# Kernel tuning notes

Measured on AMD Instinct MI355X. Metric: run time of the kernel, lower is better.

Reference implementation:

```python
import jax, jax.numpy as jnp
import numpy as np

B, C, N = 4, 512, 4096
CQK = C // 8

def setup_inputs() -> dict:
    key = jax.random.key(0)
    ks = jax.random.split(key, 8)
    s = 0.02  # weight init scale
    return {
        "x": jax.random.normal(ks[0], (B, C, N), dtype=jnp.float32),
        "Wq": jax.random.normal(ks[1], (CQK, C), dtype=jnp.float32) * s,
        "bq": jax.random.normal(ks[2], (CQK,), dtype=jnp.float32) * s,
        "Wk": jax.random.normal(ks[3], (CQK, C), dtype=jnp.float32) * s,
        "bk": jax.random.normal(ks[4], (CQK,), dtype=jnp.float32) * s,
        "Wv": jax.random.normal(ks[5], (C, C), dtype=jnp.float32) * s,
        "bv": jax.random.normal(ks[6], (C,), dtype=jnp.float32) * s,
        "gamma": jax.random.normal(ks[7], (1,), dtype=jnp.float32),
    }

def reference(x, Wq, bq, Wk, bk, Wv, bv, gamma):
    # pointwise Conv1d == per-point matmul: [B,C,N] -> [B,Cout,N]
    q = jnp.einsum('oc,bcn->bon', Wq, x) + bq[None, :, None]   # [B,CQK,N]
    k = jnp.einsum('oc,bcn->bon', Wk, x) + bk[None, :, None]   # [B,CQK,N]
    v = jnp.einsum('oc,bcn->bon', Wv, x) + bv[None, :, None]   # [B,C,N]
    # attention[b,i,j] = sum_c q[b,c,i] * k[b,c,j]  (unscaled, non-causal)
    attn = jnp.einsum('bci,bcj->bij', q, k)                    # [B,N,N]
    attn = jax.nn.softmax(attn, axis=-1)
    # out[b,c,i] = sum_j v[b,c,j] * attn[b,i,j]
    out = jnp.einsum('bcj,bij->bci', v, attn)                  # [B,C,N]
    return gamma[0] * out + x
```

## Files before the change

### kernel.cpp

```cpp
#include <hip/hip_runtime.h>
#include <math.h>

#define B_ 4
#define C_ 512
#define N_ 4096
#define LOG2E 1.44269504088896f

typedef __attribute__((ext_vector_type(8))) short s8v;
typedef __attribute__((ext_vector_type(4))) float f4v;

#define MF32(a, b, c) __builtin_amdgcn_mfma_f32_16x16x32_bf16(a, b, c, 0, 0, 0)

#if defined(__has_builtin) && __has_builtin(__builtin_amdgcn_exp2f)
#define EXP2(x) __builtin_amdgcn_exp2f(x)
#else
#define EXP2(x) exp2f(x)
#endif

#define BARRIER_LDS() do {                                   \
    __builtin_amdgcn_sched_barrier(0);                       \
    asm volatile("s_waitcnt lgkmcnt(0)" ::: "memory");       \
    __builtin_amdgcn_s_barrier();                            \
    __builtin_amdgcn_sched_barrier(0);                       \
} while (0)

static __device__ __forceinline__ ushort f2bf(float f) {
    unsigned u = __float_as_uint(f);
    u += 0x7FFFu + ((u >> 16) & 1u);
    return (ushort)(u >> 16);
}
static __device__ __forceinline__ unsigned pack2bf(float a, float b) {
    unsigned ua = __float_as_uint(a); ua += 0x7FFFu + ((ua >> 16) & 1u);
    unsigned ub = __float_as_uint(b); ub += 0x7FFFu + ((ub >> 16) & 1u);
    return (ua >> 16) | (ub & 0xffff0000u);
}

__global__ __launch_bounds__(256) void wconv_kernel(
    const float* __restrict__ Wq, const float* __restrict__ Wk,
    const float* __restrict__ Wv, ushort* __restrict__ Wb)
{
    const int row = blockIdx.x;
    const float* src = row < 64 ? Wq + (size_t)row * C_
                     : row < 128 ? Wk + (size_t)(row - 64) * C_
                     : Wv + (size_t)(row - 128) * C_;
    const int t2 = threadIdx.x * 2;
    float2 v = *(const float2*)&src[t2];
    ushort2 o; o.x = f2bf(v.x); o.y = f2bf(v.y);
    *(ushort2*)&Wb[(size_t)row * C_ + t2] = o;
}

__global__ __launch_bounds__(512, 2) void qkv_fused(
    const float* __restrict__ x, const ushort* __restrict__ Wb,
    const float* __restrict__ bq, const float* __restrict__ bk,
    const float* __restrict__ bv,
    ushort* __restrict__ qT, ushort* __restrict__ kT, ushort* __restrict__ vB)
{
    extern __shared__ ushort Xs[];

    const int tid = threadIdx.x, w = tid >> 6, lane = tid & 63;
    const int li = lane & 15, qd = lane >> 4;
    const int n0 = blockIdx.x * 64, b = blockIdx.y;

    #pragma unroll
    for (int r = 0; r < 16; ++r) {
        const int f = r * 512 + tid;
        const int c = f >> 4;
        const int nch = f & 15;
        float4 v = *(const float4*)&x[((size_t)b * C_ + c) * N_ + n0 + nch * 4];
        const int n = nch * 4;
        Xs[((n + 0) * 512 + c) ^ (((n + 0) & 7) << 3)] = f2bf(v.x);
        Xs[((n + 1) * 512 + c) ^ (((n + 1) & 7) << 3)] = f2bf(v.y);
        Xs[((n + 2) * 512 + c) ^ (((n + 2) & 7) << 3)] = f2bf(v.z);
        Xs[((n + 3) * 512 + c) ^ (((n + 3) & 7) << 3)] = f2bf(v.w);
    }
    __syncthreads();

    const int rb0 = w * 80;
    const ushort* wrow[5];
    #pragma unroll
    for (int ot = 0; ot < 5; ++ot)
        wrow[ot] = Wb + (size_t)(rb0 + ot * 16 + li) * C_ + qd * 8;

    f4v acc[5][4];
    #pragma unroll
    for (int ot = 0; ot < 5; ++ot)
        #pragma unroll
        for (int nt = 0; nt < 4; ++nt)
            acc[ot][nt] = (f4v){0.f, 0.f, 0.f, 0.f};

    s8v awc[5], awn[5];
    #pragma unroll
    for (int ot = 0; ot < 5; ++ot)
        awc[ot] = *(const s8v*)(wrow[ot]);

    #pragma unroll 1
    for (int kc = 0; kc < C_; kc += 32) {
        const int kn = (kc + 32 < C_) ? kc + 32 : 0;
        #pragma unroll
        for (int ot = 0; ot < 5; ++ot)
            awn[ot] = *(const s8v*)(wrow[ot] + kn);

        s8v bx[4];
        #pragma unroll
        for (int nt = 0; nt < 4; ++nt) {
            const int n = nt * 16 + li;
            bx[nt] = *(const s8v*)&Xs[((n * 512) + kc + qd * 8) ^ ((li & 7) << 3)];
        }

        #pragma unroll
        for (int ot = 0; ot < 5; ++ot) {
            if (rb0 + ot * 16 >= 128) {
                #pragma unroll
                for (int nt = 0; nt < 4; ++nt)
                    acc[ot][nt] = MF32(bx[nt], awc[ot], acc[ot][nt]);
            } else {
                #pragma unroll
                for (int nt = 0; nt < 4; ++nt)
                    acc[ot][nt] = MF32(awc[ot], bx[nt], acc[ot][nt]);
            }
        }
        #pragma unroll
        for (int ot = 0; ot < 5; ++ot) awc[ot] = awn[ot];
    }

    #pragma unroll
    for (int ot = 0; ot < 5; ++ot) {
        const int rb = rb0 + ot * 16;
        if (rb < 128) {
            ushort* dst = rb < 64 ? qT : kT;
            const float* bias = rb < 64 ? bq : bk;
            const int ob = (rb < 64 ? rb : rb - 64) + qd * 4;
            const float sc = rb < 64 ? LOG2E : 1.0f;
            #pragma unroll
            for (int nt = 0; nt < 4; ++nt) {
                const int n = n0 + nt * 16 + li;
                ushort4 o;
                o.x = f2bf((acc[ot][nt][0] + bias[ob + 0]) * sc);
                o.y = f2bf((acc[ot][nt][1] + bias[ob + 1]) * sc);
                o.z = f2bf((acc[ot][nt][2] + bias[ob + 2]) * sc);
                o.w = f2bf((acc[ot][nt][3] + bias[ob + 3]) * sc);
                *(ushort4*)&dst[((size_t)b * N_ + n) * 64 + ob] = o;
            }
        } else {
            const int c = rb - 128 + li;
            const float bb = bv[c];
            #pragma unroll
            for (int nt = 0; nt < 4; ++nt) {
                const int n = n0 + nt * 16 + qd * 4;
                ushort4 o;
                o.x = f2bf(acc[ot][nt][0] + bb);
                o.y = f2bf(acc[ot][nt][1] + bb);
                o.z = f2bf(acc[ot][nt][2] + bb);
                o.w = f2bf(acc[ot][nt][3] + bb);
                *(ushort4*)&vB[((size_t)b * C_ + c) * N_ + n] = o;
            }
        }
    }
}

__device__ __forceinline__ void pv_chunk(
    const ushort* __restrict__ Pr, int li, int qd, int cidx,
    const s8v* vf, f4v (&acc)[4][8])
{
    const int sw = li & 7;
    #pragma unroll
    for (int h = 0; h < 2; ++h) {
        s8v pf[4];
        #pragma unroll
        for (int g = 0; g < 4; ++g)
            pf[g] = *(const s8v*)&Pr[(size_t)((h * 4 + g) * 16 + li) * 128
                                     + (((cidx * 4 + qd) ^ sw) << 3)];
        #pragma unroll
        for (int ct = 0; ct < 4; ++ct)
            #pragma unroll
            for (int g = 0; g < 4; ++g)
                acc[ct][h * 4 + g] = MF32(vf[ct], pf[g], acc[ct][h * 4 + g]);
    }
}

__device__ __forceinline__ void s_phase(
    s8v ck0, s8v ck1, const s8v (&qf)[8][2], float (&lp)[8],
    ushort* __restrict__ Pw, int li, int qd, int chunkbase)
{
    const int off = (qd & 1) * 4;
    const int sw = li & 7;
    #pragma unroll
    for (int h = 0; h < 2; ++h) {
        f4v sac[4];
        #pragma unroll
        for (int g = 0; g < 4; ++g) {
            const int it = h * 4 + g;
            sac[g] = (f4v){0.f, 0.f, 0.f, 0.f};
            sac[g] = MF32(ck0, qf[it][0], sac[g]);
            sac[g] = MF32(ck1, qf[it][1], sac[g]);
        }
        #pragma unroll
        for (int g = 0; g < 4; ++g) {
            const int it = h * 4 + g;
            const float p0 = EXP2(sac[g][0]);
            const float p1 = EXP2(sac[g][1]);
            const float p2 = EXP2(sac[g][2]);
            const float p3 = EXP2(sac[g][3]);
            lp[it] += (p0 + p1) + (p2 + p3);
            uint2 u; u.x = pack2bf(p0, p1); u.y = pack2bf(p2, p3);
            *(uint2*)&Pw[(size_t)(it * 16 + li) * 128
                         + ((chunkbase ^ sw) << 3) + off] = u;
        }
    }
}

__global__ __launch_bounds__(512, 2) void attn_mfma(
    const ushort* __restrict__ qT, const ushort* __restrict__ kT,
    const ushort* __restrict__ vB, const float* __restrict__ x,
    const float* __restrict__ gamma, float* __restrict__ out)
{
    extern __shared__ char smem[];
    ushort* Pb0 = (ushort*)smem;
    ushort* Pb1 = (ushort*)(smem + 32768);
    float*  l_s = (float*)(smem + 65536);

    const int tid = threadIdx.x, w = tid >> 6, lane = tid & 63;
    const int li = lane & 15, qd = lane >> 4;
    const int wg = blockIdx.x;
    const int i_base = (wg >> 3) * 128;
    const int combo = wg & 7;
    const int b = combo >> 1;
    const int c_base = (combo & 1) * 256;

    const ushort* qTb = qT + (size_t)b * N_ * 64;
    const ushort* kTb = kT + (size_t)b * N_ * 64;
    const ushort* vBb = vB + (size_t)b * C_ * N_;

    if (w < 4) {
        s8v qf[8][2];
        #pragma unroll
        for (int it = 0; it < 8; ++it)
            #pragma unroll
            for (int ks = 0; ks < 2; ++ks)
                qf[it][ks] = *(const s8v*)&qTb[(size_t)(i_base + it * 16 + li) * 64 + ks * 32 + qd * 8];
        float lp[8] = {0.f, 0.f, 0.f, 0.f, 0.f, 0.f, 0.f, 0.f};

        const ushort* kptrA = kTb + (size_t)(w * 32 + li) * 64 + qd * 8;
        const ushort* kptrB = kTb + (size_t)(w * 32 + 16 + li) * 64 + qd * 8;
        const int cbA = w * 4 + (qd >> 1);
        const int cbB = w * 4 + 2 + (qd >> 1);

        s8v ka0 = *(const s8v*)(kptrA);
        s8v ka1 = *(const s8v*)(kptrA + 32);
        s8v kb0 = *(const s8v*)(kptrB);
        s8v kb1 = *(const s8v*)(kptrB + 32);
        s8v na0 = *(const s8v*)(kptrA + (size_t)128 * 64);
        s8v na1 = *(const s8v*)(kptrA + (size_t)128 * 64 + 32);
        s8v nb0 = *(const s8v*)(kptrB + (size_t)128 * 64);
        s8v nb1 = *(const s8v*)(kptrB + (size_t)128 * 64 + 32);
        s_phase(ka0, ka1, qf, lp, Pb0, li, qd, cbA);
        s_phase(kb0, kb1, qf, lp, Pb0, li, qd, cbB);
        BARRIER_LDS();

        #pragma unroll 1
        for (int t = 1; t < N_ / 128; ++t) {
            ushort* Pw = ((t - 1) & 1) ? Pb0 : Pb1;
            const size_t jnext = (t + 1 < N_ / 128) ? (size_t)(t + 1) * 128 : 0;
            s8v ca0 = na0, ca1 = na1, cb0 = nb0, cb1 = nb1;
            na0 = *(const s8v*)(kptrA + jnext * 64);
            na1 = *(const s8v*)(kptrA + jnext * 64 + 32);
            nb0 = *(const s8v*)(kptrB + jnext * 64);
            nb1 = *(const s8v*)(kptrB + jnext * 64 + 32);
            s_phase(ca0, ca1, qf, lp, Pw, li, qd, cbA);
            s_phase(cb0, cb1, qf, lp, Pw, li, qd, cbB);
            BARRIER_LDS();
        }

        #pragma unroll
        for (int it = 0; it < 8; ++it) {
            lp[it] += __shfl_xor(lp[it], 16, 64);
            lp[it] += __shfl_xor(lp[it], 32, 64);
        }
        if (qd == 0) {
            #pragma unroll
            for (int it = 0; it < 8; ++it) l_s[w * 128 + it * 16 + li] = lp[it];
        }
        BARRIER_LDS();
    } else {
        const int w2c = w - 4;
        f4v acc[4][8];
        #pragma unroll
        for (int ct = 0; ct < 4; ++ct)
            #pragma unroll
            for (int it = 0; it < 8; ++it)
                acc[ct][it] = (f4v){0.f, 0.f, 0.f, 0.f};

        const ushort* vptr[4];
        #pragma unroll
        for (int ct = 0; ct < 4; ++ct)
            vptr[ct] = vBb + (size_t)(c_base + w2c * 64 + ct * 16 + li) * N_ + qd * 8;

        s8v vcur[8];
        #pragma unroll
        for (int ch = 0; ch < 2; ++ch)
            #pragma unroll
            for (int ct = 0; ct < 4; ++ct)
                vcur[ch * 4 + ct] = *(const s8v*)(vptr[ct] + ch * 32);
        BARRIER_LDS();

        #pragma unroll 1
        for (int t = 1; t < N_ / 128; ++t) {
            const ushort* Pr = ((t - 1) & 1) ? Pb1 : Pb0;
            const size_t jprev = (size_t)(t - 1) * 128;
            const size_t jcur  = (size_t)t * 128;

            __builtin_amdgcn_s_setprio(1);
            s8v vlt0[4], vlt1[4], vnx[8];
            #pragma unroll
            for (int ct = 0; ct < 4; ++ct)
                vlt0[ct] = *(const s8v*)(vptr[ct] + jprev + 2 * 32);
            pv_chunk(Pr, li, qd, 0, &vcur[0], acc);
            #pragma unroll
            for (int ct = 0; ct < 4; ++ct)
                vlt1[ct] = *(const s8v*)(vptr[ct] + jprev + 3 * 32);
            pv_chunk(Pr, li, qd, 1, &vcur[4], acc);
            #pragma unroll
            for (int ct = 0; ct < 4; ++ct)
                vnx[ct] = *(const s8v*)(vptr[ct] + jcur);
            pv_chunk(Pr, li, qd, 2, vlt0, acc);
            #pragma unroll
            for (int ct = 0; ct < 4; ++ct)
                vnx[4 + ct] = *(const s8v*)(vptr[ct] + jcur + 32);
            pv_chunk(Pr, li, qd, 3, vlt1, acc);
            __builtin_amdgcn_s_setprio(0);

            #pragma unroll
            for (int k = 0; k < 8; ++k) vcur[k] = vnx[k];
            BARRIER_LDS();
        }

        {
            const ushort* Pr = ((N_ / 128 - 1) & 1) ? Pb1 : Pb0;
            const size_t jprev = (size_t)(N_ / 128 - 1) * 128;
            s8v vlt0[4], vlt1[4];
            #pragma unroll
            for (int ct = 0; ct < 4; ++ct)
                vlt0[ct] = *(const s8v*)(vptr[ct] + jprev + 2 * 32);
            pv_chunk(Pr, li, qd, 0, &vcur[0], acc);
            #pragma unroll
            for (int ct = 0; ct < 4; ++ct)
                vlt1[ct] = *(const s8v*)(vptr[ct] + jprev + 3 * 32);
            pv_chunk(Pr, li, qd, 1, &vcur[4], acc);
            pv_chunk(Pr, li, qd, 2, vlt0, acc);
            pv_chunk(Pr, li, qd, 3, vlt1, acc);
        }
        BARRIER_LDS();

        float inv[8];
        #pragma unroll
        for (int it = 0; it < 8; ++it) {
            float t = 0.f;
            #pragma unroll
            for (int ww = 0; ww < 4; ++ww) t += l_s[ww * 128 + it * 16 + li];
            inv[it] = 1.0f / t;
        }

        const float g = gamma[0];
        #pragma unroll
        for (int ct = 0; ct < 4; ++ct)
            #pragma unroll
            for (int it = 0; it < 8; ++it) {
                const int i = i_base + it * 16 + li;
                #pragma unroll
                for (int r = 0; r < 4; ++r) {
                    const int c = c_base + w2c * 64 + ct * 16 + qd * 4 + r;
                    const size_t off = ((size_t)b * C_ + c) * N_ + i;
                    out[off] = g * acc[ct][it][r] * inv[it] + x[off];
                }
            }
    }
}

extern "C" void kernel_launch(void* const* d_in, const int* in_sizes, int n_in,
                              void* d_out, int out_size, void* d_ws, size_t ws_size,
                              hipStream_t stream)
{
    const float* x     = (const float*)d_in[0];
    const float* Wq    = (const float*)d_in[1];
    const float* bq    = (const float*)d_in[2];
    const float* Wk    = (const float*)d_in[3];
    const float* bk    = (const float*)d_in[4];
    const float* Wv    = (const float*)d_in[5];
    const float* bv    = (const float*)d_in[6];
    const float* gamma = (const float*)d_in[7];
    float* out = (float*)d_out;

    ushort* vB = (ushort*)d_ws;
    ushort* qT = vB + (size_t)B_ * C_ * N_;
    ushort* kT = qT + (size_t)B_ * N_ * 64;
    ushort* Wb = kT + (size_t)B_ * N_ * 64;

    wconv_kernel<<<dim3(640), 256, 0, stream>>>(Wq, Wk, Wv, Wb);
    qkv_fused<<<dim3(N_ / 64, B_), 512, 65536, stream>>>(x, Wb, bq, bk, bv, qT, kT, vB);
    attn_mfma<<<dim3((N_ / 128) * 2 * B_), 512, 69632, stream>>>(qT, kT, vB, x, gamma, out);
}
```

Measured before the change: 212.3 us.

## Double the attention key tile to 256 and rotate V register prefetch

Measured after the change: 205.4 us. 3.3% less time.

```diff
diff --git a/kernel.cpp b/kernel.cpp
--- a/kernel.cpp
+++ b/kernel.cpp
@@ -168,7 +168,7 @@
         s8v pf[4];
         #pragma unroll
         for (int g = 0; g < 4; ++g)
-            pf[g] = *(const s8v*)&Pr[(size_t)((h * 4 + g) * 16 + li) * 128
+            pf[g] = *(const s8v*)&Pr[(size_t)((h * 4 + g) * 16 + li) * 256
                                      + (((cidx * 4 + qd) ^ sw) << 3)];
         #pragma unroll
         for (int ct = 0; ct < 4; ++ct)
@@ -203,7 +203,7 @@
             const float p3 = EXP2(sac[g][3]);
             lp[it] += (p0 + p1) + (p2 + p3);
             uint2 u; u.x = pack2bf(p0, p1); u.y = pack2bf(p2, p3);
-            *(uint2*)&Pw[(size_t)(it * 16 + li) * 128
+            *(uint2*)&Pw[(size_t)(it * 16 + li) * 256
                          + ((chunkbase ^ sw) << 3) + off] = u;
         }
     }
@@ -216,8 +216,8 @@
 {
     extern __shared__ char smem[];
     ushort* Pb0 = (ushort*)smem;
-    ushort* Pb1 = (ushort*)(smem + 32768);
-    float*  l_s = (float*)(smem + 65536);
+    ushort* Pb1 = (ushort*)(smem + 65536);
+    float*  l_s = (float*)smem;
 
     const int tid = threadIdx.x, w = tid >> 6, lane = tid & 63;
     const int li = lane & 15, qd = lane >> 4;
@@ -231,6 +231,8 @@
     const ushort* kTb = kT + (size_t)b * N_ * 64;
     const ushort* vBb = vB + (size_t)b * C_ * N_;
 
+    const int NT = N_ / 256;
+
     if (w < 4) {
         s8v qf[8][2];
         #pragma unroll
@@ -240,34 +242,44 @@
                 qf[it][ks] = *(const s8v*)&qTb[(size_t)(i_base + it * 16 + li) * 64 + ks * 32 + qd * 8];
         float lp[8] = {0.f, 0.f, 0.f, 0.f, 0.f, 0.f, 0.f, 0.f};
 
-        const ushort* kptrA = kTb + (size_t)(w * 32 + li) * 64 + qd * 8;
-        const ushort* kptrB = kTb + (size_t)(w * 32 + 16 + li) * 64 + qd * 8;
-        const int cbA = w * 4 + (qd >> 1);
-        const int cbB = w * 4 + 2 + (qd >> 1);
-
-        s8v ka0 = *(const s8v*)(kptrA);
-        s8v ka1 = *(const s8v*)(kptrA + 32);
-        s8v kb0 = *(const s8v*)(kptrB);
-        s8v kb1 = *(const s8v*)(kptrB + 32);
-        s8v na0 = *(const s8v*)(kptrA + (size_t)128 * 64);
-        s8v na1 = *(const s8v*)(kptrA + (size_t)128 * 64 + 32);
-        s8v nb0 = *(const s8v*)(kptrB + (size_t)128 * 64);
-        s8v nb1 = *(const s8v*)(kptrB + (size_t)128 * 64 + 32);
-        s_phase(ka0, ka1, qf, lp, Pb0, li, qd, cbA);
-        s_phase(kb0, kb1, qf, lp, Pb0, li, qd, cbB);
+        const ushort* kp[4];
+        int cb[4];
+        #pragma unroll
+        for (int s = 0; s < 4; ++s) {
+            kp[s] = kTb + (size_t)(w * 64 + s * 16 + li) * 64 + qd * 8;
+            cb[s] = w * 8 + s * 2 + (qd >> 1);
+        }
+
+        s8v kn0[4], kn1[4];
+        {
+            s8v kc0[4], kc1[4];
+            #pragma unroll
+            for (int s = 0; s < 4; ++s) {
+                kc0[s] = *(const s8v*)(kp[s]);
+                kc1[s] = *(const s8v*)(kp[s] + 32);
+            }
+            #pragma unroll
+            for (int s = 0; s < 4; ++s) {
+                kn0[s] = *(const s8v*)(kp[s] + (size_t)256 * 64);
+                kn1[s] = *(const s8v*)(kp[s] + (size_t)256 * 64 + 32);
+            }
+            #pragma unroll
+            for (int s = 0; s < 4; ++s)
+                s_phase(kc0[s], kc1[s], qf, lp, Pb0, li, qd, cb[s]);
+        }
         BARRIER_LDS();
 
         #pragma unroll 1
-        for (int t = 1; t < N_ / 128; ++t) {
+        for (int t = 1; t < NT; ++t) {
             ushort* Pw = ((t - 1) & 1) ? Pb0 : Pb1;
-            const size_t jnext = (t + 1 < N_ / 128) ? (size_t)(t + 1) * 128 : 0;
-            s8v ca0 = na0, ca1 = na1, cb0 = nb0, cb1 = nb1;
-            na0 = *(const s8v*)(kptrA + jnext * 64);
-            na1 = *(const s8v*)(kptrA + jnext * 64 + 32);
-            nb0 = *(const s8v*)(kptrB + jnext * 64);
-            nb1 = *(const s8v*)(kptrB + jnext * 64 + 32);
-            s_phase(ca0, ca1, qf, lp, Pw, li, qd, cbA);
-            s_phase(cb0, cb1, qf, lp, Pw, li, qd, cbB);
+            const size_t jnext = (t + 1 < NT) ? (size_t)(t + 1) * 256 : 0;
+            #pragma unroll
+            for (int s = 0; s < 4; ++s) {
+                s8v c0 = kn0[s], c1 = kn1[s];
+                kn0[s] = *(const s8v*)(kp[s] + jnext * 64);
+                kn1[s] = *(const s8v*)(kp[s] + jnext * 64 + 32);
+                s_phase(c0, c1, qf, lp, Pw, li, qd, cb[s]);
+            }
             BARRIER_LDS();
         }
 
@@ -295,59 +307,49 @@
         for (int ct = 0; ct < 4; ++ct)
             vptr[ct] = vBb + (size_t)(c_base + w2c * 64 + ct * 16 + li) * N_ + qd * 8;
 
-        s8v vcur[8];
-        #pragma unroll
-        for (int ch = 0; ch < 2; ++ch)
+        s8v vr[2][4];
+        #pragma unroll
+        for (int sl = 0; sl < 2; ++sl)
             #pragma unroll
             for (int ct = 0; ct < 4; ++ct)
-                vcur[ch * 4 + ct] = *(const s8v*)(vptr[ct] + ch * 32);
+                vr[sl][ct] = *(const s8v*)(vptr[ct] + sl * 32);
         BARRIER_LDS();
 
         #pragma unroll 1
-        for (int t = 1; t < N_ / 128; ++t) {
+        for (int t = 1; t < NT; ++t) {
             const ushort* Pr = ((t - 1) & 1) ? Pb1 : Pb0;
-            const size_t jprev = (size_t)(t - 1) * 128;
-            const size_t jcur  = (size_t)t * 128;
+            const size_t jprev = (size_t)(t - 1) * 256;
+            const size_t jcur  = (size_t)t * 256;
 
             __builtin_amdgcn_s_setprio(1);
-            s8v vlt0[4], vlt1[4], vnx[8];
-            #pragma unroll
-            for (int ct = 0; ct < 4; ++ct)
-                vlt0[ct] = *(const s8v*)(vptr[ct] + jprev + 2 * 32);
-            pv_chunk(Pr, li, qd, 0, &vcur[0], acc);
-            #pragma unroll
-            for (int ct = 0; ct < 4; ++ct)
-                vlt1[ct] = *(const s8v*)(vptr[ct] + jprev + 3 * 32);
-            pv_chunk(Pr, li, qd, 1, &vcur[4], acc);
-            #pragma unroll
-            for (int ct = 0; ct < 4; ++ct)
-                vnx[ct] = *(const s8v*)(vptr[ct] + jcur);
-            pv_chunk(Pr, li, qd, 2, vlt0, acc);
-            #pragma unroll
-            for (int ct = 0; ct < 4; ++ct)
-                vnx[4 + ct] = *(const s8v*)(vptr[ct] + jcur + 32);
-            pv_chunk(Pr, li, qd, 3, vlt1, acc);
+            #pragma unroll
+            for (int c = 0; c < 8; ++c) {
+                pv_chunk(Pr, li, qd, c, vr[c & 1], acc);
+                const size_t jld = (c + 2 < 8) ? jprev + (size_t)(c + 2) * 32
+                                               : jcur + (size_t)(c + 2 - 8) * 32;
+                #pragma unroll
+                for (int ct = 0; ct < 4; ++ct)
+                    vr[c & 1][ct] = *(const s8v*)(vptr[ct] + jld);
+            }
             __builtin_amdgcn_s_setprio(0);
-
-            #pragma unroll
-            for (int k = 0; k < 8; ++k) vcur[k] = vnx[k];
             BARRIER_LDS();
         }
 
         {
-            const ushort* Pr = ((N_ / 128 - 1) & 1) ? Pb1 : Pb0;
-            const size_t jprev = (size_t)(N_ / 128 - 1) * 128;
-            s8v vlt0[4], vlt1[4];
-            #pragma unroll
-            for (int ct = 0; ct < 4; ++ct)
-                vlt0[ct] = *(const s8v*)(vptr[ct] + jprev + 2 * 32);
-            pv_chunk(Pr, li, qd, 0, &vcur[0], acc);
-            #pragma unroll
-            for (int ct = 0; ct < 4; ++ct)
-                vlt1[ct] = *(const s8v*)(vptr[ct] + jprev + 3 * 32);
-            pv_chunk(Pr, li, qd, 1, &vcur[4], acc);
-            pv_chunk(Pr, li, qd, 2, vlt0, acc);
-            pv_chunk(Pr, li, qd, 3, vlt1, acc);
+            const ushort* Pr = ((NT - 2) & 1) ? Pb0 : Pb1;
+            const size_t jprev = (size_t)(NT - 1) * 256;
+            __builtin_amdgcn_s_setprio(1);
+            #pragma unroll
+            for (int c = 0; c < 8; ++c) {
+                pv_chunk(Pr, li, qd, c, vr[c & 1], acc);
+                if (c + 2 < 8) {
+                    const size_t jld = jprev + (size_t)(c + 2) * 32;
+                    #pragma unroll
+                    for (int ct = 0; ct < 4; ++ct)
+                        vr[c & 1][ct] = *(const s8v*)(vptr[ct] + jld);
+                }
+            }
+            __builtin_amdgcn_s_setprio(0);
         }
         BARRIER_LDS();
 
@@ -397,5 +399,5 @@
 
     wconv_kernel<<<dim3(640), 256, 0, stream>>>(Wq, Wk, Wv, Wb);
     qkv_fused<<<dim3(N_ / 64, B_), 512, 65536, stream>>>(x, Wb, bq, bk, bv, qT, kT, vB);
-    attn_mfma<<<dim3((N_ / 128) * 2 * B_), 512, 69632, stream>>>(qT, kT, vB, x, gamma, out);
-}
+    attn_mfma<<<dim3((N_ / 128) * 2 * B_), 512, 131072, stream>>>(qT, kT, vB, x, gamma, out);
+}
```
